# Kernel optimization log

Measured on AMD Instinct MI355X. Metric: run time of the kernel, lower is better.

## Reference

```python
import jax, jax.numpy as jnp
import numpy as np

HIDDEN = 1024
HEADS = 16
DK = HIDDEN // HEADS  # 64
B, N = 2, 2048


def setup_inputs() -> dict:
    key = jax.random.key(0)
    ks = jax.random.split(key, 12)
    s = 0.02
    return {
        "q": jax.random.normal(ks[0], (B, N, HIDDEN), jnp.float32),
        "k": jax.random.normal(ks[1], (B, N, HIDDEN), jnp.float32),
        "v": jax.random.normal(ks[2], (B, N, HIDDEN), jnp.float32),
        "attn_bias": jax.random.normal(ks[3], (B, N, N), jnp.float32),
        "attention_mask": jnp.zeros((B, N, N), jnp.float32),
        # projection weights stored [in, out]
        "Wq": jax.random.normal(ks[4], (HIDDEN, HIDDEN), jnp.float32) * s,
        "bq": jnp.zeros((HIDDEN,), jnp.float32),
        "Wk": jax.random.normal(ks[5], (HIDDEN, HIDDEN), jnp.float32) * s,
        "bk": jnp.zeros((HIDDEN,), jnp.float32),
        "Wv": jax.random.normal(ks[6], (HIDDEN, HIDDEN), jnp.float32) * s,
        "bv": jnp.zeros((HIDDEN,), jnp.float32),
        "Wo": jax.random.normal(ks[7], (HIDDEN, HIDDEN), jnp.float32) * s,
        "bo": jnp.zeros((HIDDEN,), jnp.float32),
    }


def reference(q, k, v, attn_bias, attention_mask, Wq, bq, Wk, bk, Wv, bv, Wo, bo):
    b, n, _ = q.shape
    scale = DK ** (-0.5)
    # project and split heads: [B, H, N, Dk]
    qh = (q @ Wq + bq).reshape(b, n, HEADS, DK).transpose(0, 2, 1, 3)
    kh = (k @ Wk + bk).reshape(b, -1, HEADS, DK).transpose(0, 2, 1, 3)
    vh = (v @ Wv + bv).reshape(b, -1, HEADS, DK).transpose(0, 2, 1, 3)
    # scaled scores + additive bias/mask broadcast over heads: [B, H, N, N]
    scores = jnp.einsum('bhnd,bhmd->bhnm', qh * scale, kh)
    scores = scores + attn_bias[:, None, :, :] + attention_mask[:, None, :, :]
    probs = jax.nn.softmax(scores, axis=-1)  # dropout is identity at inference
    ctx = jnp.einsum('bhnm,bhmd->bhnd', probs, vh)
    ctx = ctx.transpose(0, 2, 1, 3).reshape(b, n, HEADS * DK)
    return ctx @ Wo + bo
```

## Files before the change

kernel.cpp:

```cpp
#include <hip/hip_runtime.h>
#include <hip/hip_bf16.h>

#define HIDDEN 1024
#define NHEADS 16
#define DKH   64
#define BATCH 2
#define SEQ   2048
#define MTOT  (BATCH*SEQ)

using bf16x8 = __attribute__((ext_vector_type(8))) short;
using f32x4  = __attribute__((ext_vector_type(4))) float;
using u16x4  = __attribute__((ext_vector_type(4))) unsigned short;

__device__ __forceinline__ unsigned short f2bf(float f) {
    union { __hip_bfloat16 h; unsigned short u; } v;
    v.h = __float2bfloat16(f);
    return v.u;
}

__device__ __forceinline__ float asfloat(unsigned int u) {
    union { unsigned int u; float f; } v; v.u = u; return v.f;
}

__device__ __forceinline__ float fexp2(float x) {
#if __has_builtin(__builtin_amdgcn_exp2f)
    return __builtin_amdgcn_exp2f(x);
#else
    return exp2f(x);
#endif
}

__device__ __forceinline__ void gload16(const unsigned short* g, unsigned short* l) {
    __builtin_amdgcn_global_load_lds((const __attribute__((address_space(1))) void*)g,
                                     (__attribute__((address_space(3))) void*)l, 16, 0, 0);
}

#define L2E 1.44269504088896340736f

__global__ __launch_bounds__(256) void prep(const float* __restrict__ Wq,
                                            const float* __restrict__ Wk,
                                            const float* __restrict__ Wv,
                                            const float* __restrict__ Wo,
                                            unsigned short* __restrict__ wt,
                                            const float* __restrict__ bias,
                                            const float* __restrict__ mask,
                                            unsigned short* __restrict__ biasf) {
    __shared__ __align__(16) char sh[16640];
    float (*tile)[65] = (float (*)[65])sh;
    unsigned short (*lb)[520] = (unsigned short (*)[520])sh;
    const int bid = blockIdx.x, t = threadIdx.x;
    if (bid >= 1024) {
        int r = bid - 1024;
        const int z = r >> 8; r &= 255;
        const int kb = (r >> 4) * 64, nb = (r & 15) * 64;
        const float* W = (z == 0) ? Wq : (z == 1) ? Wk : (z == 2) ? Wv : Wo;
        unsigned short* out = wt + (size_t)z * HIDDEN * HIDDEN;
        #pragma unroll
        for (int i = 0; i < 16; i++) {
            int idx = i * 256 + t; int rr = idx >> 6, c = idx & 63;
            tile[rr][c] = W[(size_t)(kb + rr) * HIDDEN + nb + c];
        }
        __syncthreads();
        #pragma unroll
        for (int i = 0; i < 16; i++) {
            int idx = i * 256 + t; int n = idx >> 6, kk = idx & 63;
            out[(size_t)(nb + n) * HIDDEN + kb + kk] = f2bf(tile[kk][n]);
        }
    } else {
        const int cb = bid;
        const int chunk = cb & 3, g = (cb >> 2) & 127, b = cb >> 9;
        const float* bp = bias + ((size_t)b * SEQ + g * 16) * SEQ + chunk * 512;
        const float* mp = mask + ((size_t)b * SEQ + g * 16) * SEQ + chunk * 512;
        #pragma unroll
        for (int i = 0; i < 8; i++) {
            int idx = i * 256 + t;
            int row = idx >> 7, c4 = (idx & 127) * 4;
            float4 bv4 = *(const float4*)(bp + (size_t)row * SEQ + c4);
            float4 mv4 = *(const float4*)(mp + (size_t)row * SEQ + c4);
            union { u16x4 v; unsigned short s[4]; } o;
            o.s[0] = f2bf((bv4.x + mv4.x) * L2E);
            o.s[1] = f2bf((bv4.y + mv4.y) * L2E);
            o.s[2] = f2bf((bv4.z + mv4.z) * L2E);
            o.s[3] = f2bf((bv4.w + mv4.w) * L2E);
            *(u16x4*)&lb[row][c4] = o.v;
        }
        __syncthreads();
        const int w = t >> 6, ln = t & 63;
        const int quad = ln >> 4, c16 = ln & 15;
        unsigned short* ob = biasf + (((size_t)b * 128 + g) * 64 + chunk * 16) * 512 + ln * 8;
        #pragma unroll
        for (int it = 0; it < 4; it++) {
            int ttl = it * 4 + w;
            *(bf16x8*)(ob + (size_t)ttl * 512) = *(const bf16x8*)&lb[c16][ttl * 32 + quad * 8];
        }
    }
}

__global__ __launch_bounds__(256, 2) void proj_gemm(const float* __restrict__ qf32,
                                                    const float* __restrict__ kf32,
                                                    const float* __restrict__ vf32,
                                                    const unsigned short* __restrict__ Wtall,
                                                    const float* __restrict__ bq,
                                                    const float* __restrict__ bk,
                                                    const float* __restrict__ bv,
                                                    unsigned short* __restrict__ qh,
                                                    unsigned short* __restrict__ khs,
                                                    unsigned short* __restrict__ vts) {
    __shared__ __align__(16) unsigned short smem[24576];
    const int z = blockIdx.z;
    const float* X  = (z == 0) ? qf32 : (z == 1) ? kf32 : vf32;
    const unsigned short* Wt = Wtall + (size_t)z * HIDDEN * HIDDEN;
    const float* bias = (z == 0) ? bq : (z == 1) ? bk : bv;
    const int mbase = blockIdx.x * 128, nbase = blockIdx.y * 128;
    const int tid = threadIdx.x, w = tid >> 6, ln = tid & 63;
    const int qr = (w >> 1) * 64, qc = (w & 1) * 64;
    const int g = ln >> 4, c16 = ln & 15;

    f32x4 acc[4][4];
    #pragma unroll
    for (int rt = 0; rt < 4; rt++)
        #pragma unroll
        for (int ct = 0; ct < 4; ct++) acc[rt][ct] = (f32x4){0.f, 0.f, 0.f, 0.f};

    float4 fa[4][2];
    #pragma unroll
    for (int pass = 0; pass < 4; pass++) {
        int L = pass * 256 + tid;
        int r = L >> 3, cc = L & 7;
        const float* p = X + (size_t)(mbase + r) * HIDDEN + cc * 8;
        fa[pass][0] = *(const float4*)p;
        fa[pass][1] = *(const float4*)(p + 4);
    }
    #pragma unroll
    for (int pass = 0; pass < 4; pass++) {
        int L = pass * 256 + tid;
        int r = L >> 3, c = (L & 7) ^ (r & 7);
        gload16(Wt + (size_t)(nbase + r) * HIDDEN + c * 8,
                smem + 8192 + (size_t)(pass * 256 + w * 64) * 8);
    }

    for (int kk = 0; kk < HIDDEN; kk += 64) {
        const int cur = (kk >> 6) & 1;
        __syncthreads();
        #pragma unroll
        for (int pass = 0; pass < 4; pass++) {
            int L = pass * 256 + tid;
            int r = L >> 3, cc = L & 7;
            int cs = cc ^ (r & 7);
            union { bf16x8 v; unsigned short s[8]; } o;
            o.s[0] = f2bf(fa[pass][0].x); o.s[1] = f2bf(fa[pass][0].y);
            o.s[2] = f2bf(fa[pass][0].z); o.s[3] = f2bf(fa[pass][0].w);
            o.s[4] = f2bf(fa[pass][1].x); o.s[5] = f2bf(fa[pass][1].y);
            o.s[6] = f2bf(fa[pass][1].z); o.s[7] = f2bf(fa[pass][1].w);
            *(bf16x8*)(smem + (size_t)(r * 8 + cs) * 8) = o.v;
        }
        __syncthreads();
        if (kk + 64 < HIDDEN) {
            #pragma unroll
            for (int pass = 0; pass < 4; pass++) {
                int L = pass * 256 + tid;
                int r = L >> 3, c = (L & 7) ^ (r & 7);
                gload16(Wt + (size_t)(nbase + r) * HIDDEN + (kk + 64) + c * 8,
                        smem + 8192 + (1 - cur) * 8192 + (size_t)(pass * 256 + w * 64) * 8);
            }
            #pragma unroll
            for (int pass = 0; pass < 4; pass++) {
                int L = pass * 256 + tid;
                int r = L >> 3, cc = L & 7;
                const float* p = X + (size_t)(mbase + r) * HIDDEN + (kk + 64) + cc * 8;
                fa[pass][0] = *(const float4*)p;
                fa[pass][1] = *(const float4*)(p + 4);
            }
        }
        const unsigned short* bbuf = smem + 8192 + cur * 8192;
        #pragma unroll
        for (int ks = 0; ks < 2; ks++) {
            bf16x8 af[4], bfr[4];
            #pragma unroll
            for (int rt = 0; rt < 4; rt++) {
                int r = qr + rt * 16 + c16;
                int ch = (g + ks * 4) ^ (r & 7);
                af[rt] = *(const bf16x8*)(smem + (size_t)(r * 8 + ch) * 8);
            }
            #pragma unroll
            for (int ct = 0; ct < 4; ct++) {
                int n = qc + ct * 16 + c16;
                int ch = (g + ks * 4) ^ (n & 7);
                bfr[ct] = *(const bf16x8*)(bbuf + (size_t)(n * 8 + ch) * 8);
            }
            #pragma unroll
            for (int rt = 0; rt < 4; rt++)
                #pragma unroll
                for (int ct = 0; ct < 4; ct++)
                    acc[rt][ct] = __builtin_amdgcn_mfma_f32_16x16x32_bf16(af[rt], bfr[ct], acc[rt][ct], 0, 0, 0);
        }
    }
    __syncthreads();

    const float scale = (z == 0) ? (0.125f * L2E) : 1.0f;
    float bias_v[4];
    #pragma unroll
    for (int ct = 0; ct < 4; ct++) bias_v[ct] = bias[nbase + qc + ct * 16 + c16];

    unsigned short* eld = smem + w * 4608;
    #pragma unroll
    for (int rt = 0; rt < 4; rt++)
        #pragma unroll
        for (int ct = 0; ct < 4; ct++)
            #pragma unroll
            for (int r4 = 0; r4 < 4; r4++) {
                int row_l = rt * 16 + g * 4 + r4;
                int col_l = ct * 16 + c16;
                float val = (acc[rt][ct][r4] + bias_v[ct]) * scale;
                if (z == 2) eld[col_l * 72 + row_l] = f2bf(val);
                else        eld[row_l * 72 + col_l] = f2bf(val);
            }
    __syncthreads();

    const int b = mbase >> 11;
    const int pos0 = (mbase & 2047) + qr;
    const int h = (nbase + qc) >> 6;
    const int bh = b * NHEADS + h;
    if (z == 0) {
        const int row8 = ln >> 3, col8 = (ln & 7) * 8;
        unsigned short* dst0 = qh + ((size_t)bh * SEQ + pos0) * DKH;
        #pragma unroll
        for (int j = 0; j < 8; j++) {
            int row = j * 8 + row8;
            *(bf16x8*)(dst0 + row * 64 + col8) = *(const bf16x8*)&eld[row * 72 + col8];
        }
    } else if (z == 1) {
        unsigned short* base = khs + ((size_t)bh * 64 + (pos0 >> 5)) * 2048;
        const int kvp = (c16 >> 2) * 8 + (c16 & 3);
        #pragma unroll
        for (int j = 0; j < 8; j++) {
            int tloc = j >> 2, ks = (j >> 1) & 1, kvs = j & 1;
            int kvl = tloc * 32 + kvp + kvs * 4;
            *(bf16x8*)(base + tloc * 2048 + ks * 1024 + kvs * 512 + ln * 8)
                = *(const bf16x8*)&eld[kvl * 72 + ks * 32 + g * 8];
        }
    } else {
        unsigned short* base = vts + ((size_t)bh * 64 + (pos0 >> 5)) * 2048;
        #pragma unroll
        for (int j = 0; j < 8; j++) {
            int tloc = j >> 2, dt = j & 3;
            *(bf16x8*)(base + tloc * 2048 + dt * 512 + ln * 8)
                = *(const bf16x8*)&eld[(dt * 16 + c16) * 72 + tloc * 32 + g * 8];
        }
    }
}

__global__ __launch_bounds__(256, 4) void attn(const unsigned short* __restrict__ qh,
                                               const unsigned short* __restrict__ khs,
                                               const unsigned short* __restrict__ vts,
                                               const unsigned short* __restrict__ biasf,
                                               unsigned short* __restrict__ ctx) {
    __shared__ __align__(16) unsigned short smem[16384];
    const int tid = threadIdx.x, w = tid >> 6, ln = tid & 63;
    const int quad = ln >> 4, c16 = ln & 15;
    const int bid = blockIdx.x;
    const int xcd = bid & 7, jj = bid >> 3;
    const int bh = xcd * 4 + (jj >> 5);
    const int qb = jj & 31;
    const int b = bh >> 4, h = bh & 15;

    bf16x8 qf[2];
    {
        const unsigned short* qp = qh + ((size_t)bh * SEQ + qb * 64 + w * 16 + c16) * DKH + quad * 8;
        qf[0] = *(const bf16x8*)qp;
        qf[1] = *(const bf16x8*)(qp + 32);
    }

    const unsigned short* kT = khs + (size_t)bh * 131072;
    const unsigned short* vT = vts + (size_t)bh * 131072;
    const unsigned short* bb = biasf + (((size_t)(b * 128 + qb * 4 + w) * 64) * 512) + ln * 8;

    const short one_bf = (short)0x3F80;
    bf16x8 vones = {one_bf, one_bf, one_bf, one_bf, one_bf, one_bf, one_bf, one_bf};

    f32x4 accv[4];
    #pragma unroll
    for (int dt = 0; dt < 4; dt++) accv[dt] = (f32x4){0.f, 0.f, 0.f, 0.f};
    f32x4 dsum = (f32x4){0.f, 0.f, 0.f, 0.f};

    bf16x8 bA[4], bB[4];
    #pragma unroll
    for (int j = 0; j < 4; j++) bA[j] = *(const bf16x8*)(bb + j * 512);

    #define HALF_TILE(T, bc, bn)                                                        \
    {                                                                                   \
        __syncthreads();                             \
        {                                                                               \
            const unsigned short* ksrc = kT + (T) * 8192 + w * 512 + ln * 8;            \
            const unsigned short* vsrc = vT + (T) * 8192 + w * 512 + ln * 8;            \
            unsigned short* lk = smem + w * 512;                                        \
            unsigned short* lv = smem + 8192 + w * 512;                                 \
            _Pragma("unroll")                                                           \
            for (int p = 0; p < 4; p++) {                                               \
                gload16(ksrc + p * 2048, lk + p * 2048);                                \
                gload16(vsrc + p * 2048, lv + p * 2048);                                \
            }                                                                           \
        }                                                                               \
        {                                                                               \
            const int Tn = ((T) < 15) ? (T) + 1 : 15;                                   \
            _Pragma("unroll")                                                           \
            for (int j = 0; j < 4; j++)                                                 \
                bn[j] = *(const bf16x8*)(bb + (size_t)(Tn * 4 + j) * 512);              \
        }                                                                               \
        __syncthreads();                                     \
        _Pragma("unroll")                                                               \
        for (int j = 0; j < 4; j++) {                                                   \
            bf16x8 kf00 = *(const bf16x8*)(smem + j * 2048 + ln * 8);                   \
            bf16x8 kf01 = *(const bf16x8*)(smem + j * 2048 + 512 + ln * 8);             \
            bf16x8 kf10 = *(const bf16x8*)(smem + j * 2048 + 1024 + ln * 8);            \
            bf16x8 kf11 = *(const bf16x8*)(smem + j * 2048 + 1536 + ln * 8);            \
            bf16x8 vf[4];                                                               \
            _Pragma("unroll")                                                           \
            for (int dt = 0; dt < 4; dt++)                                              \
                vf[dt] = *(const bf16x8*)(smem + 8192 + j * 2048 + dt * 512 + ln * 8);  \
            const unsigned int* bd = (const unsigned int*)&bc[j];                       \
            f32x4 s0, s1;                                                               \
            s0[0] = asfloat(bd[0] << 16); s0[1] = asfloat(bd[0] & 0xFFFF0000u);         \
            s0[2] = asfloat(bd[1] << 16); s0[3] = asfloat(bd[1] & 0xFFFF0000u);         \
            s1[0] = asfloat(bd[2] << 16); s1[1] = asfloat(bd[2] & 0xFFFF0000u);         \
            s1[2] = asfloat(bd[3] << 16); s1[3] = asfloat(bd[3] & 0xFFFF0000u);         \
            s0 = __builtin_amdgcn_mfma_f32_16x16x32_bf16(kf00, qf[0], s0, 0, 0, 0);     \
            s0 = __builtin_amdgcn_mfma_f32_16x16x32_bf16(kf10, qf[1], s0, 0, 0, 0);     \
            s1 = __builtin_amdgcn_mfma_f32_16x16x32_bf16(kf01, qf[0], s1, 0, 0, 0);     \
            s1 = __builtin_amdgcn_mfma_f32_16x16x32_bf16(kf11, qf[1], s1, 0, 0, 0);     \
            _Pragma("unroll")                                                           \
            for (int r = 0; r < 4; r++) { s0[r] = fexp2(s0[r]); s1[r] = fexp2(s1[r]); } \
            union { bf16x8 v; __hip_bfloat162 hh[4]; } pu;                              \
            pu.hh[0] = __float22bfloat162_rn(make_float2(s0[0], s0[1]));                \
            pu.hh[1] = __float22bfloat162_rn(make_float2(s0[2], s0[3]));                \
            pu.hh[2] = __float22bfloat162_rn(make_float2(s1[0], s1[1]));                \
            pu.hh[3] = __float22bfloat162_rn(make_float2(s1[2], s1[3]));                \
            dsum = __builtin_amdgcn_mfma_f32_16x16x32_bf16(vones, pu.v, dsum, 0, 0, 0); \
            _Pragma("unroll")                                                           \
            for (int dt = 0; dt < 4; dt++)                                              \
                accv[dt] = __builtin_amdgcn_mfma_f32_16x16x32_bf16(vf[dt], pu.v,        \
                                                                   accv[dt], 0, 0, 0); \
        }                                                                               \
    }

    for (int T = 0; T < 16; T += 2) {
        HALF_TILE(T,     bA, bB)
        HALF_TILE(T + 1, bB, bA)
    }
    #undef HALF_TILE

    const float inv = 1.0f / dsum[0];
    __syncthreads();
    unsigned short* ot = smem + w * 1152;
    #pragma unroll
    for (int dt = 0; dt < 4; dt++)
        #pragma unroll
        for (int r = 0; r < 4; r += 2) {
            union { __hip_bfloat162 hh; unsigned int u; } pk;
            pk.hh = __float22bfloat162_rn(make_float2(accv[dt][r] * inv,
                                                     accv[dt][r + 1] * inv));
            *(unsigned int*)&ot[c16 * 72 + dt * 16 + quad * 4 + r] = pk.u;
        }
    const int row = ln >> 2, seg = ln & 3;
    const unsigned short* srcp = ot + row * 72 + seg * 16;
    unsigned short* dstp = ctx + ((size_t)b * SEQ + qb * 64 + w * 16 + row) * HIDDEN
                         + h * 64 + seg * 16;
    *(bf16x8*)(dstp)     = *(const bf16x8*)(srcp);
    *(bf16x8*)(dstp + 8) = *(const bf16x8*)(srcp + 8);
}

__global__ __launch_bounds__(256, 2) void outproj(const unsigned short* __restrict__ X,
                                                  const unsigned short* __restrict__ Wt,
                                                  const float* __restrict__ bo,
                                                  float* __restrict__ out) {
    __shared__ __align__(16) unsigned short smem[12288];
    const int mbase = blockIdx.x * 64, nbase = blockIdx.y * 128;
    const int tid = threadIdx.x, w = tid >> 6, ln = tid & 63;
    const int qr = (w >> 1) * 32, qc = (w & 1) * 64;
    const int g = ln >> 4, c16 = ln & 15;

    f32x4 acc[2][4];
    #pragma unroll
    for (int rt = 0; rt < 2; rt++)
        #pragma unroll
        for (int ct = 0; ct < 4; ct++) acc[rt][ct] = (f32x4){0.f, 0.f, 0.f, 0.f};

    for (int kk = 0; kk < HIDDEN; kk += 64) {
        __syncthreads();
        #pragma unroll
        for (int pass = 0; pass < 2; pass++) {
            int L = pass * 256 + tid;
            int r = L >> 3, c = (L & 7) ^ (r & 7);
            gload16(X + (size_t)(mbase + r) * HIDDEN + kk + c * 8,
                    smem + (size_t)(pass * 256 + w * 64) * 8);
        }
        #pragma unroll
        for (int pass = 0; pass < 4; pass++) {
            int L = pass * 256 + tid;
            int r = L >> 3, c = (L & 7) ^ (r & 7);
            gload16(Wt + (size_t)(nbase + r) * HIDDEN + kk + c * 8,
                    smem + 4096 + (size_t)(pass * 256 + w * 64) * 8);
        }
        __syncthreads();
        #pragma unroll
        for (int ks = 0; ks < 2; ks++) {
            bf16x8 af[2], bfr[4];
            #pragma unroll
            for (int rt = 0; rt < 2; rt++) {
                int r = qr + rt * 16 + c16;
                int ch = (g + ks * 4) ^ (r & 7);
                af[rt] = *(const bf16x8*)(smem + (size_t)(r * 8 + ch) * 8);
            }
            #pragma unroll
            for (int ct = 0; ct < 4; ct++) {
                int n = qc + ct * 16 + c16;
                int ch = (g + ks * 4) ^ (n & 7);
                bfr[ct] = *(const bf16x8*)(smem + 4096 + (size_t)(n * 8 + ch) * 8);
            }
            #pragma unroll
            for (int rt = 0; rt < 2; rt++)
                #pragma unroll
                for (int ct = 0; ct < 4; ct++)
                    acc[rt][ct] = __builtin_amdgcn_mfma_f32_16x16x32_bf16(af[rt], bfr[ct], acc[rt][ct], 0, 0, 0);
        }
    }

    float bo_v[4];
    #pragma unroll
    for (int ct = 0; ct < 4; ct++) bo_v[ct] = bo[nbase + qc + ct * 16 + c16];
    #pragma unroll
    for (int rt = 0; rt < 2; rt++)
        #pragma unroll
        for (int ct = 0; ct < 4; ct++)
            #pragma unroll
            for (int r4 = 0; r4 < 4; r4++)
                out[(size_t)(mbase + qr + rt * 16 + g * 4 + r4) * HIDDEN + nbase + qc + ct * 16 + c16]
                    = acc[rt][ct][r4] + bo_v[ct];
}

extern "C" void kernel_launch(void* const* d_in, const int* in_sizes, int n_in,
                              void* d_out, int out_size, void* d_ws, size_t ws_size,
                              hipStream_t stream) {
    const float* q    = (const float*)d_in[0];
    const float* k    = (const float*)d_in[1];
    const float* v    = (const float*)d_in[2];
    const float* bias = (const float*)d_in[3];
    const float* mask = (const float*)d_in[4];
    const float* Wq   = (const float*)d_in[5];
    const float* bq   = (const float*)d_in[6];
    const float* Wk   = (const float*)d_in[7];
    const float* bk   = (const float*)d_in[8];
    const float* Wv   = (const float*)d_in[9];
    const float* bv   = (const float*)d_in[10];
    const float* Wo   = (const float*)d_in[11];
    const float* bo   = (const float*)d_in[12];

    char* ws = (char*)d_ws;
    unsigned short* biasf  = (unsigned short*)ws;
    unsigned short* wt     = (unsigned short*)(ws + 16777216);
    unsigned short* qh     = (unsigned short*)(ws + 25165824);
    unsigned short* khs    = (unsigned short*)(ws + 33554432);
    unsigned short* vts    = (unsigned short*)(ws + 41943040);
    unsigned short* ctx    = (unsigned short*)(ws + 50331648);

    prep<<<2048, 256, 0, stream>>>(Wq, Wk, Wv, Wo, wt, bias, mask, biasf);
    proj_gemm<<<dim3(32, 8, 3), 256, 0, stream>>>(q, k, v, wt, bq, bk, bv, qh, khs, vts);
    attn<<<1024, 256, 0, stream>>>(qh, khs, vts, biasf, ctx);
    outproj<<<dim3(64, 8), 256, 0, stream>>>(ctx, wt + (size_t)3 * HIDDEN * HIDDEN, bo,
                                             (float*)d_out);
}
```

Baseline: 275.5 us.

## Pair two heads per attention block and single-buffer projection weight tiles

The attention kernel now launches 512-thread blocks, each covering the same query tile for two adjacent heads. Each half of the block has its own LDS region, so the paired heads read the same attn_bias rows at the same time, which should improve cache reuse of the bias stream. Separately, the QKV projection GEMM drops double-buffering of the weight tile and loads it at the top of each k-step. This lowers LDS use, but the weight load no longer overlaps with the MFMA work.

```diff
diff --git a/kernel.cpp b/kernel.cpp
--- a/kernel.cpp
+++ b/kernel.cpp
@@ -106,7 +106,7 @@
                                                     unsigned short* __restrict__ qh,
                                                     unsigned short* __restrict__ khs,
                                                     unsigned short* __restrict__ vts) {
-    __shared__ __align__(16) unsigned short smem[24576];
+    __shared__ __align__(16) unsigned short smem[18432];
     const int z = blockIdx.z;
     const float* X  = (z == 0) ? qf32 : (z == 1) ? kf32 : vf32;
     const unsigned short* Wt = Wtall + (size_t)z * HIDDEN * HIDDEN;
@@ -131,17 +131,16 @@
         fa[pass][0] = *(const float4*)p;
         fa[pass][1] = *(const float4*)(p + 4);
     }
-    #pragma unroll
-    for (int pass = 0; pass < 4; pass++) {
-        int L = pass * 256 + tid;
-        int r = L >> 3, c = (L & 7) ^ (r & 7);
-        gload16(Wt + (size_t)(nbase + r) * HIDDEN + c * 8,
-                smem + 8192 + (size_t)(pass * 256 + w * 64) * 8);
-    }
 
     for (int kk = 0; kk < HIDDEN; kk += 64) {
-        const int cur = (kk >> 6) & 1;
-        __syncthreads();
+        __syncthreads();
+        #pragma unroll
+        for (int pass = 0; pass < 4; pass++) {
+            int L = pass * 256 + tid;
+            int r = L >> 3, c = (L & 7) ^ (r & 7);
+            gload16(Wt + (size_t)(nbase + r) * HIDDEN + kk + c * 8,
+                    smem + 8192 + (size_t)(pass * 256 + w * 64) * 8);
+        }
         #pragma unroll
         for (int pass = 0; pass < 4; pass++) {
             int L = pass * 256 + tid;
@@ -159,20 +158,12 @@
             #pragma unroll
             for (int pass = 0; pass < 4; pass++) {
                 int L = pass * 256 + tid;
-                int r = L >> 3, c = (L & 7) ^ (r & 7);
-                gload16(Wt + (size_t)(nbase + r) * HIDDEN + (kk + 64) + c * 8,
-                        smem + 8192 + (1 - cur) * 8192 + (size_t)(pass * 256 + w * 64) * 8);
-            }
-            #pragma unroll
-            for (int pass = 0; pass < 4; pass++) {
-                int L = pass * 256 + tid;
                 int r = L >> 3, cc = L & 7;
                 const float* p = X + (size_t)(mbase + r) * HIDDEN + (kk + 64) + cc * 8;
                 fa[pass][0] = *(const float4*)p;
                 fa[pass][1] = *(const float4*)(p + 4);
             }
         }
-        const unsigned short* bbuf = smem + 8192 + cur * 8192;
         #pragma unroll
         for (int ks = 0; ks < 2; ks++) {
             bf16x8 af[4], bfr[4];
@@ -186,7 +177,7 @@
             for (int ct = 0; ct < 4; ct++) {
                 int n = qc + ct * 16 + c16;
                 int ch = (g + ks * 4) ^ (n & 7);
-                bfr[ct] = *(const bf16x8*)(bbuf + (size_t)(n * 8 + ch) * 8);
+                bfr[ct] = *(const bf16x8*)(smem + 8192 + (size_t)(n * 8 + ch) * 8);
             }
             #pragma unroll
             for (int rt = 0; rt < 4; rt++)
@@ -250,30 +241,34 @@
     }
 }
 
-__global__ __launch_bounds__(256, 4) void attn(const unsigned short* __restrict__ qh,
+__global__ __launch_bounds__(512, 4) void attn(const unsigned short* __restrict__ qh,
                                                const unsigned short* __restrict__ khs,
                                                const unsigned short* __restrict__ vts,
                                                const unsigned short* __restrict__ biasf,
                                                unsigned short* __restrict__ ctx) {
-    __shared__ __align__(16) unsigned short smem[16384];
+    __shared__ __align__(16) unsigned short smem[32768];
     const int tid = threadIdx.x, w = tid >> 6, ln = tid & 63;
+    const int w4 = w & 3, hh = w >> 2;
     const int quad = ln >> 4, c16 = ln & 15;
     const int bid = blockIdx.x;
     const int xcd = bid & 7, jj = bid >> 3;
-    const int bh = xcd * 4 + (jj >> 5);
+    const int hp = xcd * 2 + (jj >> 5);
     const int qb = jj & 31;
-    const int b = bh >> 4, h = bh & 15;
+    const int b = hp >> 3, h = (hp & 7) * 2 + hh;
+    const int bh = b * NHEADS + h;
+
+    unsigned short* mysmem = smem + hh * 16384;
 
     bf16x8 qf[2];
     {
-        const unsigned short* qp = qh + ((size_t)bh * SEQ + qb * 64 + w * 16 + c16) * DKH + quad * 8;
+        const unsigned short* qp = qh + ((size_t)bh * SEQ + qb * 64 + w4 * 16 + c16) * DKH + quad * 8;
         qf[0] = *(const bf16x8*)qp;
         qf[1] = *(const bf16x8*)(qp + 32);
     }
 
     const unsigned short* kT = khs + (size_t)bh * 131072;
     const unsigned short* vT = vts + (size_t)bh * 131072;
-    const unsigned short* bb = biasf + (((size_t)(b * 128 + qb * 4 + w) * 64) * 512) + ln * 8;
+    const unsigned short* bb = biasf + (((size_t)(b * 128 + qb * 4 + w4) * 64) * 512) + ln * 8;
 
     const short one_bf = (short)0x3F80;
     bf16x8 vones = {one_bf, one_bf, one_bf, one_bf, one_bf, one_bf, one_bf, one_bf};
@@ -291,10 +286,10 @@
     {                                                                                   \
         __syncthreads();                             \
         {                                                                               \
-            const unsigned short* ksrc = kT + (T) * 8192 + w * 512 + ln * 8;            \
-            const unsigned short* vsrc = vT + (T) * 8192 + w * 512 + ln * 8;            \
-            unsigned short* lk = smem + w * 512;                                        \
-            unsigned short* lv = smem + 8192 + w * 512;                                 \
+            const unsigned short* ksrc = kT + (T) * 8192 + w4 * 512 + ln * 8;           \
+            const unsigned short* vsrc = vT + (T) * 8192 + w4 * 512 + ln * 8;           \
+            unsigned short* lk = mysmem + w4 * 512;                                     \
+            unsigned short* lv = mysmem + 8192 + w4 * 512;                              \
             _Pragma("unroll")                                                           \
             for (int p = 0; p < 4; p++) {                                               \
                 gload16(ksrc + p * 2048, lk + p * 2048);                                \
@@ -310,14 +305,14 @@
         __syncthreads();                                     \
         _Pragma("unroll")                                                               \
         for (int j = 0; j < 4; j++) {                                                   \
-            bf16x8 kf00 = *(const bf16x8*)(smem + j * 2048 + ln * 8);                   \
-            bf16x8 kf01 = *(const bf16x8*)(smem + j * 2048 + 512 + ln * 8);             \
-            bf16x8 kf10 = *(const bf16x8*)(smem + j * 2048 + 1024 + ln * 8);            \
-            bf16x8 kf11 = *(const bf16x8*)(smem + j * 2048 + 1536 + ln * 8);            \
+            bf16x8 kf00 = *(const bf16x8*)(mysmem + j * 2048 + ln * 8);                 \
+            bf16x8 kf01 = *(const bf16x8*)(mysmem + j * 2048 + 512 + ln * 8);           \
+            bf16x8 kf10 = *(const bf16x8*)(mysmem + j * 2048 + 1024 + ln * 8);          \
+            bf16x8 kf11 = *(const bf16x8*)(mysmem + j * 2048 + 1536 + ln * 8);          \
             bf16x8 vf[4];                                                               \
             _Pragma("unroll")                                                           \
             for (int dt = 0; dt < 4; dt++)                                              \
-                vf[dt] = *(const bf16x8*)(smem + 8192 + j * 2048 + dt * 512 + ln * 8);  \
+                vf[dt] = *(const bf16x8*)(mysmem + 8192 + j * 2048 + dt * 512 + ln * 8);\
             const unsigned int* bd = (const unsigned int*)&bc[j];                       \
             f32x4 s0, s1;                                                               \
             s0[0] = asfloat(bd[0] << 16); s0[1] = asfloat(bd[0] & 0xFFFF0000u);         \
@@ -330,11 +325,11 @@
             s1 = __builtin_amdgcn_mfma_f32_16x16x32_bf16(kf11, qf[1], s1, 0, 0, 0);     \
             _Pragma("unroll")                                                           \
             for (int r = 0; r < 4; r++) { s0[r] = fexp2(s0[r]); s1[r] = fexp2(s1[r]); } \
-            union { bf16x8 v; __hip_bfloat162 hh[4]; } pu;                              \
-            pu.hh[0] = __float22bfloat162_rn(make_float2(s0[0], s0[1]));                \
-            pu.hh[1] = __float22bfloat162_rn(make_float2(s0[2], s0[3]));                \
-            pu.hh[2] = __float22bfloat162_rn(make_float2(s1[0], s1[1]));                \
-            pu.hh[3] = __float22bfloat162_rn(make_float2(s1[2], s1[3]));                \
+            union { bf16x8 v; __hip_bfloat162 hh2[4]; } pu;                             \
+            pu.hh2[0] = __float22bfloat162_rn(make_float2(s0[0], s0[1]));               \
+            pu.hh2[1] = __float22bfloat162_rn(make_float2(s0[2], s0[3]));               \
+            pu.hh2[2] = __float22bfloat162_rn(make_float2(s1[0], s1[1]));               \
+            pu.hh2[3] = __float22bfloat162_rn(make_float2(s1[2], s1[3]));               \
             dsum = __builtin_amdgcn_mfma_f32_16x16x32_bf16(vones, pu.v, dsum, 0, 0, 0); \
             _Pragma("unroll")                                                           \
             for (int dt = 0; dt < 4; dt++)                                              \
@@ -356,14 +351,14 @@
     for (int dt = 0; dt < 4; dt++)
         #pragma unroll
         for (int r = 0; r < 4; r += 2) {
-            union { __hip_bfloat162 hh; unsigned int u; } pk;
-            pk.hh = __float22bfloat162_rn(make_float2(accv[dt][r] * inv,
-                                                     accv[dt][r + 1] * inv));
+            union { __hip_bfloat162 hhp; unsigned int u; } pk;
+            pk.hhp = __float22bfloat162_rn(make_float2(accv[dt][r] * inv,
+                                                      accv[dt][r + 1] * inv));
             *(unsigned int*)&ot[c16 * 72 + dt * 16 + quad * 4 + r] = pk.u;
         }
     const int row = ln >> 2, seg = ln & 3;
     const unsigned short* srcp = ot + row * 72 + seg * 16;
-    unsigned short* dstp = ctx + ((size_t)b * SEQ + qb * 64 + w * 16 + row) * HIDDEN
+    unsigned short* dstp = ctx + ((size_t)b * SEQ + qb * 64 + w4 * 16 + row) * HIDDEN
                          + h * 64 + seg * 16;
     *(bf16x8*)(dstp)     = *(const bf16x8*)(srcp);
     *(bf16x8*)(dstp + 8) = *(const bf16x8*)(srcp + 8);
@@ -465,7 +460,7 @@
 
     prep<<<2048, 256, 0, stream>>>(Wq, Wk, Wv, Wo, wt, bias, mask, biasf);
     proj_gemm<<<dim3(32, 8, 3), 256, 0, stream>>>(q, k, v, wt, bq, bk, bv, qh, khs, vts);
-    attn<<<1024, 256, 0, stream>>>(qh, khs, vts, biasf, ctx);
+    attn<<<512, 512, 0, stream>>>(qh, khs, vts, biasf, ctx);
     outproj<<<dim3(64, 8), 256, 0, stream>>>(ctx, wt + (size_t)3 * HIDDEN * HIDDEN, bo,
                                              (float*)d_out);
 }
```

Measured after the change: 276.4 us. About the same (+0.3%).

## Move bias/mask conversion into projection GEMM grid and single-buffer weight tiles

Applied to the files above, without the earlier changes.

The bias+mask to bf16 conversion blocks move out of the prep kernel and become extra z-slices of the projection GEMM launch. Their bandwidth-heavy work can then overlap with the compute-bound GEMM blocks, and prep shrinks to the weight transpose only. The GEMM's B-tile double buffer is replaced with a single buffer loaded at the top of each k-step, cutting LDS from 48KB to 36KB. The cost is that the weight loads are no longer prefetched one step ahead and now sit exposed before the MFMA work.

```diff
diff --git a/kernel.cpp b/kernel.cpp
--- a/kernel.cpp
+++ b/kernel.cpp
@@ -41,39 +41,53 @@
                                             const float* __restrict__ Wk,
                                             const float* __restrict__ Wv,
                                             const float* __restrict__ Wo,
-                                            unsigned short* __restrict__ wt,
-                                            const float* __restrict__ bias,
-                                            const float* __restrict__ mask,
-                                            unsigned short* __restrict__ biasf) {
-    __shared__ __align__(16) char sh[16640];
-    float (*tile)[65] = (float (*)[65])sh;
-    unsigned short (*lb)[520] = (unsigned short (*)[520])sh;
-    const int bid = blockIdx.x, t = threadIdx.x;
-    if (bid >= 1024) {
-        int r = bid - 1024;
-        const int z = r >> 8; r &= 255;
-        const int kb = (r >> 4) * 64, nb = (r & 15) * 64;
-        const float* W = (z == 0) ? Wq : (z == 1) ? Wk : (z == 2) ? Wv : Wo;
-        unsigned short* out = wt + (size_t)z * HIDDEN * HIDDEN;
-        #pragma unroll
-        for (int i = 0; i < 16; i++) {
-            int idx = i * 256 + t; int rr = idx >> 6, c = idx & 63;
-            tile[rr][c] = W[(size_t)(kb + rr) * HIDDEN + nb + c];
-        }
-        __syncthreads();
-        #pragma unroll
-        for (int i = 0; i < 16; i++) {
-            int idx = i * 256 + t; int n = idx >> 6, kk = idx & 63;
-            out[(size_t)(nb + n) * HIDDEN + kb + kk] = f2bf(tile[kk][n]);
-        }
-    } else {
-        const int cb = bid;
-        const int chunk = cb & 3, g = (cb >> 2) & 127, b = cb >> 9;
-        const float* bp = bias + ((size_t)b * SEQ + g * 16) * SEQ + chunk * 512;
-        const float* mp = mask + ((size_t)b * SEQ + g * 16) * SEQ + chunk * 512;
+                                            unsigned short* __restrict__ wt) {
+    __shared__ float tile[64][65];
+    int r = blockIdx.x;
+    const int t = threadIdx.x;
+    const int z = r >> 8; r &= 255;
+    const int kb = (r >> 4) * 64, nb = (r & 15) * 64;
+    const float* W = (z == 0) ? Wq : (z == 1) ? Wk : (z == 2) ? Wv : Wo;
+    unsigned short* out = wt + (size_t)z * HIDDEN * HIDDEN;
+    #pragma unroll
+    for (int i = 0; i < 16; i++) {
+        int idx = i * 256 + t; int rr = idx >> 6, c = idx & 63;
+        tile[rr][c] = W[(size_t)(kb + rr) * HIDDEN + nb + c];
+    }
+    __syncthreads();
+    #pragma unroll
+    for (int i = 0; i < 16; i++) {
+        int idx = i * 256 + t; int n = idx >> 6, kk = idx & 63;
+        out[(size_t)(nb + n) * HIDDEN + kb + kk] = f2bf(tile[kk][n]);
+    }
+}
+
+__global__ __launch_bounds__(256, 2) void proj_gemm(const float* __restrict__ qf32,
+                                                    const float* __restrict__ kf32,
+                                                    const float* __restrict__ vf32,
+                                                    const unsigned short* __restrict__ Wtall,
+                                                    const float* __restrict__ bq,
+                                                    const float* __restrict__ bk,
+                                                    const float* __restrict__ bv,
+                                                    unsigned short* __restrict__ qh,
+                                                    unsigned short* __restrict__ khs,
+                                                    unsigned short* __restrict__ vts,
+                                                    const float* __restrict__ bias,
+                                                    const float* __restrict__ mask,
+                                                    unsigned short* __restrict__ biasf) {
+    __shared__ __align__(16) unsigned short smem[18432];
+    const int z = blockIdx.z;
+    const int tid = threadIdx.x;
+
+    if (z >= 3) {
+        const int cb = (z - 3) * 256 + blockIdx.y * 32 + blockIdx.x;
+        const int chunk = cb & 3, g2 = (cb >> 2) & 127, b2 = cb >> 9;
+        unsigned short (*lb)[520] = (unsigned short (*)[520])smem;
+        const float* bp = bias + ((size_t)b2 * SEQ + g2 * 16) * SEQ + chunk * 512;
+        const float* mp = mask + ((size_t)b2 * SEQ + g2 * 16) * SEQ + chunk * 512;
         #pragma unroll
         for (int i = 0; i < 8; i++) {
-            int idx = i * 256 + t;
+            int idx = i * 256 + tid;
             int row = idx >> 7, c4 = (idx & 127) * 4;
             float4 bv4 = *(const float4*)(bp + (size_t)row * SEQ + c4);
             float4 mv4 = *(const float4*)(mp + (size_t)row * SEQ + c4);
@@ -85,34 +99,22 @@
             *(u16x4*)&lb[row][c4] = o.v;
         }
         __syncthreads();
-        const int w = t >> 6, ln = t & 63;
-        const int quad = ln >> 4, c16 = ln & 15;
-        unsigned short* ob = biasf + (((size_t)b * 128 + g) * 64 + chunk * 16) * 512 + ln * 8;
+        const int w2 = tid >> 6, ln2 = tid & 63;
+        const int quad2 = ln2 >> 4, c162 = ln2 & 15;
+        unsigned short* ob = biasf + (((size_t)b2 * 128 + g2) * 64 + chunk * 16) * 512 + ln2 * 8;
         #pragma unroll
         for (int it = 0; it < 4; it++) {
-            int ttl = it * 4 + w;
-            *(bf16x8*)(ob + (size_t)ttl * 512) = *(const bf16x8*)&lb[c16][ttl * 32 + quad * 8];
-        }
-    }
-}
-
-__global__ __launch_bounds__(256, 2) void proj_gemm(const float* __restrict__ qf32,
-                                                    const float* __restrict__ kf32,
-                                                    const float* __restrict__ vf32,
-                                                    const unsigned short* __restrict__ Wtall,
-                                                    const float* __restrict__ bq,
-                                                    const float* __restrict__ bk,
-                                                    const float* __restrict__ bv,
-                                                    unsigned short* __restrict__ qh,
-                                                    unsigned short* __restrict__ khs,
-                                                    unsigned short* __restrict__ vts) {
-    __shared__ __align__(16) unsigned short smem[24576];
-    const int z = blockIdx.z;
+            int ttl = it * 4 + w2;
+            *(bf16x8*)(ob + (size_t)ttl * 512) = *(const bf16x8*)&lb[c162][ttl * 32 + quad2 * 8];
+        }
+        return;
+    }
+
     const float* X  = (z == 0) ? qf32 : (z == 1) ? kf32 : vf32;
     const unsigned short* Wt = Wtall + (size_t)z * HIDDEN * HIDDEN;
-    const float* bias = (z == 0) ? bq : (z == 1) ? bk : bv;
+    const float* bvec = (z == 0) ? bq : (z == 1) ? bk : bv;
     const int mbase = blockIdx.x * 128, nbase = blockIdx.y * 128;
-    const int tid = threadIdx.x, w = tid >> 6, ln = tid & 63;
+    const int w = tid >> 6, ln = tid & 63;
     const int qr = (w >> 1) * 64, qc = (w & 1) * 64;
     const int g = ln >> 4, c16 = ln & 15;
 
@@ -131,17 +133,16 @@
         fa[pass][0] = *(const float4*)p;
         fa[pass][1] = *(const float4*)(p + 4);
     }
-    #pragma unroll
-    for (int pass = 0; pass < 4; pass++) {
-        int L = pass * 256 + tid;
-        int r = L >> 3, c = (L & 7) ^ (r & 7);
-        gload16(Wt + (size_t)(nbase + r) * HIDDEN + c * 8,
-                smem + 8192 + (size_t)(pass * 256 + w * 64) * 8);
-    }
 
     for (int kk = 0; kk < HIDDEN; kk += 64) {
-        const int cur = (kk >> 6) & 1;
         __syncthreads();
+        #pragma unroll
+        for (int pass = 0; pass < 4; pass++) {
+            int L = pass * 256 + tid;
+            int r = L >> 3, c = (L & 7) ^ (r & 7);
+            gload16(Wt + (size_t)(nbase + r) * HIDDEN + kk + c * 8,
+                    smem + 8192 + (size_t)(pass * 256 + w * 64) * 8);
+        }
         #pragma unroll
         for (int pass = 0; pass < 4; pass++) {
             int L = pass * 256 + tid;
@@ -159,20 +160,12 @@
             #pragma unroll
             for (int pass = 0; pass < 4; pass++) {
                 int L = pass * 256 + tid;
-                int r = L >> 3, c = (L & 7) ^ (r & 7);
-                gload16(Wt + (size_t)(nbase + r) * HIDDEN + (kk + 64) + c * 8,
-                        smem + 8192 + (1 - cur) * 8192 + (size_t)(pass * 256 + w * 64) * 8);
-            }
-            #pragma unroll
-            for (int pass = 0; pass < 4; pass++) {
-                int L = pass * 256 + tid;
                 int r = L >> 3, cc = L & 7;
                 const float* p = X + (size_t)(mbase + r) * HIDDEN + (kk + 64) + cc * 8;
                 fa[pass][0] = *(const float4*)p;
                 fa[pass][1] = *(const float4*)(p + 4);
             }
         }
-        const unsigned short* bbuf = smem + 8192 + cur * 8192;
         #pragma unroll
         for (int ks = 0; ks < 2; ks++) {
             bf16x8 af[4], bfr[4];
@@ -186,7 +179,7 @@
             for (int ct = 0; ct < 4; ct++) {
                 int n = qc + ct * 16 + c16;
                 int ch = (g + ks * 4) ^ (n & 7);
-                bfr[ct] = *(const bf16x8*)(bbuf + (size_t)(n * 8 + ch) * 8);
+                bfr[ct] = *(const bf16x8*)(smem + 8192 + (size_t)(n * 8 + ch) * 8);
             }
             #pragma unroll
             for (int rt = 0; rt < 4; rt++)
@@ -200,7 +193,7 @@
     const float scale = (z == 0) ? (0.125f * L2E) : 1.0f;
     float bias_v[4];
     #pragma unroll
-    for (int ct = 0; ct < 4; ct++) bias_v[ct] = bias[nbase + qc + ct * 16 + c16];
+    for (int ct = 0; ct < 4; ct++) bias_v[ct] = bvec[nbase + qc + ct * 16 + c16];
 
     unsigned short* eld = smem + w * 4608;
     #pragma unroll
@@ -463,8 +456,9 @@
     unsigned short* vts    = (unsigned short*)(ws + 41943040);
     unsigned short* ctx    = (unsigned short*)(ws + 50331648);
 
-    prep<<<2048, 256, 0, stream>>>(Wq, Wk, Wv, Wo, wt, bias, mask, biasf);
-    proj_gemm<<<dim3(32, 8, 3), 256, 0, stream>>>(q, k, v, wt, bq, bk, bv, qh, khs, vts);
+    prep<<<1024, 256, 0, stream>>>(Wq, Wk, Wv, Wo, wt);
+    proj_gemm<<<dim3(32, 8, 7), 256, 0, stream>>>(q, k, v, wt, bq, bk, bv,
+                                                  qh, khs, vts, bias, mask, biasf);
     attn<<<1024, 256, 0, stream>>>(qh, khs, vts, biasf, ctx);
     outproj<<<dim3(64, 8), 256, 0, stream>>>(ctx, wt + (size_t)3 * HIDDEN * HIDDEN, bo,
                                              (float*)d_out);
```

After: 267.5 us. -2.9%, faster.
